# Kernel tuning notes

Hardware: AMD Instinct MI355X
Metric: run time of the kernel (lower is better)

The kernel has to match this reference:

```python
import jax, jax.numpy as jnp
import numpy as np

N_USERS = 100000
N_ITEMS = 50000
N_NODES = N_USERS + N_ITEMS
EMB = 64
NNZ = 6000000
N_LAYERS = 3


def setup_inputs() -> dict:
    key = jax.random.key(0)
    k1, k2, k3, k4, k5 = jax.random.split(key, 5)
    user_emb = jax.random.normal(k1, (N_USERS, EMB), dtype=jnp.float32) * 0.1
    item_emb = jax.random.normal(k2, (N_ITEMS, EMB), dtype=jnp.float32) * 0.1
    adj_rows = jax.random.randint(k3, (NNZ,), 0, N_NODES, dtype=jnp.int32)
    adj_cols = jax.random.randint(k4, (NNZ,), 0, N_NODES, dtype=jnp.int32)
    # normalized adjacency values (positive, small, like 1/sqrt(d_i d_j))
    adj_vals = jax.random.uniform(k5, (NNZ,), dtype=jnp.float32) * 0.05
    return {"user_emb": user_emb, "item_emb": item_emb,
            "adj_rows": adj_rows, "adj_cols": adj_cols, "adj_vals": adj_vals}


def _spmm(rows, cols, vals, x):
    # sparse [N,N] @ dense [N,D] via gather + segment_sum
    msgs = vals[:, None] * x[cols]                      # [nnz, D]
    return jax.ops.segment_sum(msgs, rows, num_segments=N_NODES)


def reference(user_emb, item_emb, adj_rows, adj_cols, adj_vals):
    emb = jnp.concatenate([user_emb, item_emb], axis=0)  # [N, D]
    all_emb = [emb]
    for _ in range(N_LAYERS):
        emb = _spmm(adj_rows, adj_cols, adj_vals, emb)
        all_emb.append(emb)
    stacked = jnp.stack(all_emb)                         # [L+1, N, D]
    final_emb = stacked.mean(axis=0)                     # [N, D]
    return (final_emb[:N_USERS], final_emb[N_USERS:], stacked)
```

## Files before the change

### kernel.cpp

```cpp
#include <hip/hip_runtime.h>
#include <hip/hip_bf16.h>


constexpr int N_USERS = 100000;
constexpr int N_ITEMS = 50000;
constexpr int N_NODES = N_USERS + N_ITEMS;
constexpr int EMB     = 64;
constexpr int NNZ     = 6000000;
constexpr long long NODE_ELEMS = (long long)N_NODES * EMB;
constexpr float SCALE     = 64.0f;
constexpr float INV_SCALE = 1.0f / 64.0f;
constexpr float VMAX      = 0.05f;
constexpr float VENC      = 16383.0f / VMAX;
constexpr float VDEC      = VMAX / 16383.0f;

constexpr int BSHIFT = 10;
constexpr int BROWS  = 1 << BSHIFT;
constexpr int NBUCK  = (N_NODES + BROWS - 1) / BROWS;

constexpr int COPY_BLOCKS = (int)((NODE_ELEMS / 4 + 255) / 256);
constexpr int HIST_EPT = 16;
constexpr int HIST_BLOCKS = (NNZ + 256 * HIST_EPT - 1) / (256 * HIST_EPT);

__device__ __forceinline__ unsigned int enc_fp8x4(float a, float b, float c, float d) {
    int r = 0;
    r = __builtin_amdgcn_cvt_pk_fp8_f32(a, b, r, false);
    r = __builtin_amdgcn_cvt_pk_fp8_f32(c, d, r, true);
    return (unsigned int)r;
}
__device__ __forceinline__ float4 dec_fp8x4(unsigned int u) {
    auto lo = __builtin_amdgcn_cvt_pk_f32_fp8((int)u, false);
    auto hi = __builtin_amdgcn_cvt_pk_f32_fp8((int)u, true);
    return make_float4(lo[0], lo[1], hi[0], hi[1]);
}

__global__ void zero_buckets_kernel(int* __restrict__ p) {
    int t = threadIdx.x;
    if (t < NBUCK) p[t] = 0;
}

__global__ void copy_hist_kernel(const float* __restrict__ user_emb,
                                 const float* __restrict__ item_emb,
                                 float* __restrict__ slot0,
                                 unsigned int* __restrict__ xq0,
                                 const int* __restrict__ rows,
                                 int* __restrict__ bucket_cnt) {
    if (blockIdx.x < COPY_BLOCKS) {
        long long i4 = (long long)blockIdx.x * 256 + threadIdx.x;
        long long n4 = NODE_ELEMS / 4;
        if (i4 >= n4) return;
        long long i = i4 * 4;
        const long long user_elems = (long long)N_USERS * EMB;
        float4 v;
        if (i < user_elems) {
            v = *reinterpret_cast<const float4*>(user_emb + i);
        } else {
            v = *reinterpret_cast<const float4*>(item_emb + (i - user_elems));
        }
        *reinterpret_cast<float4*>(slot0 + i) = v;
        xq0[i4] = enc_fp8x4(v.x * SCALE, v.y * SCALE, v.z * SCALE, v.w * SCALE);
    } else {
        __shared__ int lcnt[NBUCK];
        int bid = blockIdx.x - COPY_BLOCKS;
        int tid = threadIdx.x;
        for (int i = tid; i < NBUCK; i += 256) lcnt[i] = 0;
        __syncthreads();
        long long base = (long long)bid * 256 * HIST_EPT;
        for (int k = 0; k < HIST_EPT; ++k) {
            long long e = base + (long long)k * 256 + tid;
            if (e < NNZ) atomicAdd(&lcnt[rows[e] >> BSHIFT], 1);
        }
        __syncthreads();
        for (int i = tid; i < NBUCK; i += 256) {
            int c = lcnt[i];
            if (c) atomicAdd(&bucket_cnt[i], c);
        }
    }
}

__global__ void bucket_scan_kernel(const int* __restrict__ bucket_cnt,
                                   int* __restrict__ bucket_base,
                                   int* __restrict__ bucket_cursor,
                                   int* __restrict__ row_ptr) {
    __shared__ int s[256];
    int t = threadIdx.x;
    s[t] = (t < NBUCK) ? bucket_cnt[t] : 0;
    __syncthreads();
    int orig = s[t];
    for (int off = 1; off < 256; off <<= 1) {
        int v = (t >= off) ? s[t - off] : 0;
        __syncthreads();
        s[t] += v;
        __syncthreads();
    }
    int excl = s[t] - orig;
    if (t < NBUCK) {
        bucket_base[t] = excl;
        bucket_cursor[t] = excl;
    }
    if (t == NBUCK - 1) bucket_base[NBUCK] = s[t];
    if (t == 0) row_ptr[N_NODES] = NNZ;
}

constexpr int PART_T   = 1024;
constexpr int PART_EPT = 16;
__global__ __launch_bounds__(PART_T) void partition_kernel(
        const int* __restrict__ rows,
        const int* __restrict__ cols,
        const float* __restrict__ vals,
        int* __restrict__ bucket_cursor,
        unsigned long long* __restrict__ part) {
    __shared__ int lcnt[NBUCK];
    __shared__ int lcur[NBUCK];
    int tid = threadIdx.x;
    for (int i = tid; i < NBUCK; i += PART_T) lcnt[i] = 0;
    __syncthreads();
    long long tbase = (long long)blockIdx.x * PART_T * PART_EPT;
    int rloc[PART_EPT];
#pragma unroll
    for (int k = 0; k < PART_EPT; ++k) {
        long long e = tbase + (long long)k * PART_T + tid;
        int r = (e < NNZ) ? rows[e] : -1;
        rloc[k] = r;
        if (r >= 0) atomicAdd(&lcnt[r >> BSHIFT], 1);
    }
    __syncthreads();
    for (int i = tid; i < NBUCK; i += PART_T) {
        lcur[i] = atomicAdd(&bucket_cursor[i], lcnt[i]);
    }
    __syncthreads();
#pragma unroll
    for (int k = 0; k < PART_EPT; ++k) {
        int r = rloc[k];
        if (r < 0) continue;
        long long e = tbase + (long long)k * PART_T + tid;
        int b = r >> BSHIFT;
        int pos = atomicAdd(&lcur[b], 1);
        unsigned int w0 = ((unsigned int)(r & (BROWS - 1)) << 18) | (unsigned int)cols[e];
        unsigned int q = (unsigned int)(int)(fminf(fmaxf(vals[e] * VENC + 0.5f, 0.0f), 16383.0f));
        part[pos] = ((unsigned long long)q << 32) | (unsigned long long)w0;
    }
}

__global__ __launch_bounds__(BROWS) void bucket_sort_kernel(
        const int* __restrict__ bucket_base,
        const unsigned long long* __restrict__ part,
        int* __restrict__ row_ptr,
        unsigned int* __restrict__ col_val) {
    __shared__ int lcnt[BROWS];
    __shared__ int lcur[BROWS];
    int b = blockIdx.x;
    int t = threadIdx.x;
    int base = bucket_base[b];
    int n    = bucket_base[b + 1] - base;
    lcnt[t] = 0;
    __syncthreads();
    for (int j = t; j < n; j += BROWS) {
        unsigned int w0 = (unsigned int)part[base + j];
        atomicAdd(&lcnt[w0 >> 18], 1);
    }
    __syncthreads();
    int orig = lcnt[t];
    for (int off = 1; off < BROWS; off <<= 1) {
        int v = (t >= off) ? lcnt[t - off] : 0;
        __syncthreads();
        lcnt[t] += v;
        __syncthreads();
    }
    int excl = lcnt[t] - orig;
    int gr = b * BROWS + t;
    if (gr < N_NODES) row_ptr[gr] = base + excl;
    lcur[t] = base + excl;
    __syncthreads();
    for (int j = t; j < n; j += BROWS) {
        unsigned long long w = part[base + j];
        unsigned int w0 = (unsigned int)w;
        unsigned int q  = (unsigned int)(w >> 32);
        int rowoff = (int)(w0 >> 18);
        unsigned int col = w0 & 0x3FFFFu;
        int pos = atomicAdd(&lcur[rowoff], 1);
        col_val[pos] = (col << 14) | q;
    }
}

__global__ void spmm_fp8_kernel(const int* __restrict__ row_ptr,
                                const unsigned int* __restrict__ col_val,
                                const unsigned int* __restrict__ xq_in,
                                float* __restrict__ y,
                                unsigned int* __restrict__ xq_out,
                                const float4* __restrict__ s0,
                                const float4* __restrict__ s1,
                                const float4* __restrict__ s2,
                                float4* __restrict__ fin) {
    int row = blockIdx.x * (blockDim.x >> 6) + (threadIdx.x >> 6);
    int lane = threadIdx.x & 63;
    int g  = lane >> 4;
    int d4 = lane & 15;
    if (row >= N_NODES) return;
    int s = row_ptr[row];
    int e = row_ptr[row + 1];
    float4 acc = make_float4(0.f, 0.f, 0.f, 0.f);
    int i = s;
    for (; i + 32 <= e; i += 32) {
        unsigned int cv[8];
        unsigned int q[8];
#pragma unroll
        for (int k = 0; k < 8; ++k) cv[k] = col_val[i + 4 * k + g];
#pragma unroll
        for (int k = 0; k < 8; ++k) q[k] = xq_in[((cv[k] >> 14) << 4) | d4];
#pragma unroll
        for (int k = 0; k < 8; ++k) {
            float v = (float)(cv[k] & 0x3FFFu) * VDEC;
            float4 x = dec_fp8x4(q[k]);
            acc.x += v * x.x; acc.y += v * x.y; acc.z += v * x.z; acc.w += v * x.w;
        }
    }
    for (; i < e; i += 16) {
        unsigned int cv[4];
        unsigned int q[4];
#pragma unroll
        for (int k = 0; k < 4; ++k) {
            int idx = i + 4 * k + g;
            cv[k] = (idx < e) ? col_val[idx] : 0u;
        }
#pragma unroll
        for (int k = 0; k < 4; ++k) q[k] = xq_in[((cv[k] >> 14) << 4) | d4];
#pragma unroll
        for (int k = 0; k < 4; ++k) {
            float v = (float)(cv[k] & 0x3FFFu) * VDEC;
            float4 x = dec_fp8x4(q[k]);
            acc.x += v * x.x; acc.y += v * x.y; acc.z += v * x.z; acc.w += v * x.w;
        }
    }
    acc.x += __shfl_xor(acc.x, 16); acc.y += __shfl_xor(acc.y, 16);
    acc.z += __shfl_xor(acc.z, 16); acc.w += __shfl_xor(acc.w, 16);
    acc.x += __shfl_xor(acc.x, 32); acc.y += __shfl_xor(acc.y, 32);
    acc.z += __shfl_xor(acc.z, 32); acc.w += __shfl_xor(acc.w, 32);
    if (g == 0) {
        long long o = (long long)row * 16 + d4;
        float4 r;
        r.x = acc.x * INV_SCALE;
        r.y = acc.y * INV_SCALE;
        r.z = acc.z * INV_SCALE;
        r.w = acc.w * INV_SCALE;
        reinterpret_cast<float4*>(y)[o] = r;
        if (xq_out) xq_out[o] = enc_fp8x4(acc.x, acc.y, acc.z, acc.w);
        if (fin) {
            float4 a = s0[o], b = s1[o], c = s2[o];
            float4 f;
            f.x = (a.x + b.x + c.x + r.x) * 0.25f;
            f.y = (a.y + b.y + c.y + r.y) * 0.25f;
            f.z = (a.z + b.z + c.z + r.z) * 0.25f;
            f.w = (a.w + b.w + c.w + r.w) * 0.25f;
            fin[o] = f;
        }
    }
}

extern "C" void kernel_launch(void* const* d_in, const int* in_sizes, int n_in,
                              void* d_out, int out_size, void* d_ws, size_t ws_size,
                              hipStream_t stream) {
    const float* user_emb = (const float*)d_in[0];
    const float* item_emb = (const float*)d_in[1];
    const int*   adj_rows = (const int*)d_in[2];
    const int*   adj_cols = (const int*)d_in[3];
    const float* adj_vals = (const float*)d_in[4];

    float* out = (float*)d_out;
    float* final_emb = out;
    float* stacked   = out + NODE_ELEMS;
    float* slot[4];
    for (int l = 0; l < 4; ++l) slot[l] = stacked + (long long)l * NODE_ELEMS;

    unsigned long long* part = (unsigned long long*)slot[1];

    size_t off = 0;
    auto carve = [&](size_t bytes) { size_t o = off; off += (bytes + 15) & ~(size_t)15; return o; };
    size_t o_rp = carve((size_t)(N_NODES + 1) * 4);
    size_t o_cv = carve((size_t)NNZ * 4);
    size_t o_bc = carve((size_t)NBUCK * 4);
    size_t o_bb = carve((size_t)(NBUCK + 1) * 4);
    size_t o_bu = carve((size_t)NBUCK * 4);
    size_t o_x0 = carve((size_t)(NODE_ELEMS / 4) * 4);
    size_t o_x1 = carve((size_t)(NODE_ELEMS / 4) * 4);
    char* ws = (char*)d_ws;
    int*          row_ptr       = (int*)(ws + o_rp);
    unsigned int* col_val       = (unsigned int*)(ws + o_cv);
    int*          bucket_cnt    = (int*)(ws + o_bc);
    int*          bucket_base   = (int*)(ws + o_bb);
    int*          bucket_cursor = (int*)(ws + o_bu);
    unsigned int* xq[2];
    xq[0] = (unsigned int*)(ws + o_x0);
    xq[1] = (unsigned int*)(ws + o_x1);

    const int B = 256;

    zero_buckets_kernel<<<1, 256, 0, stream>>>(bucket_cnt);
    copy_hist_kernel<<<COPY_BLOCKS + HIST_BLOCKS, B, 0, stream>>>(
        user_emb, item_emb, slot[0], xq[0], adj_rows, bucket_cnt);

    bucket_scan_kernel<<<1, 256, 0, stream>>>(bucket_cnt, bucket_base, bucket_cursor, row_ptr);
    const int part_grid = (NNZ + PART_T * PART_EPT - 1) / (PART_T * PART_EPT);
    partition_kernel<<<part_grid, PART_T, 0, stream>>>(
        adj_rows, adj_cols, adj_vals, bucket_cursor, part);
    bucket_sort_kernel<<<NBUCK, BROWS, 0, stream>>>(bucket_base, part, row_ptr, col_val);

    const int rows_per_block = B / 64;
    const int grid_spmm = (N_NODES + rows_per_block - 1) / rows_per_block;
    for (int l = 0; l < 3; ++l) {
        unsigned int* xq_in  = xq[l & 1];
        unsigned int* xq_out = (l < 2) ? xq[(l + 1) & 1] : nullptr;
        bool last = (l == 2);
        spmm_fp8_kernel<<<grid_spmm, B, 0, stream>>>(
            row_ptr, col_val, xq_in, slot[l + 1], xq_out,
            last ? (const float4*)slot[0] : nullptr,
            last ? (const float4*)slot[1] : nullptr,
            last ? (const float4*)slot[2] : nullptr,
            last ? (float4*)final_emb : nullptr);
    }
}
```

Before: 479.5 us.

## Split CSR rows into column bands and run SpMM as persistent column-phased blocks

The bucket sort now orders each row's nonzeros by column band (five bands of 32K columns) and writes per-row, per-band pointers. The SpMM is replaced by a persistent kernel of 512 blocks, each owning a contiguous range of rows with accumulators in shared memory. Blocks sweep the column bands in phase, so the gathered fp8 embedding working set at any time is a fraction of the table and is meant to stay cache resident. In exchange, each row is processed in up to five short segments with reductions per segment, there is only one wave per row at a time, and load balance becomes static.

New measurement: 945.7 us. +97.2%, slower.

```diff
diff --git a/kernel.cpp b/kernel.cpp
--- a/kernel.cpp
+++ b/kernel.cpp
@@ -17,6 +17,9 @@
 constexpr int BSHIFT = 10;
 constexpr int BROWS  = 1 << BSHIFT;
 constexpr int NBUCK  = (N_NODES + BROWS - 1) / BROWS;
+
+constexpr int NQ     = 5;
+constexpr int QSHIFT = 15;
 
 constexpr int COPY_BLOCKS = (int)((NODE_ELEMS / 4 + 255) / 256);
 constexpr int HIST_EPT = 16;
@@ -81,7 +84,7 @@
 __global__ void bucket_scan_kernel(const int* __restrict__ bucket_cnt,
                                    int* __restrict__ bucket_base,
                                    int* __restrict__ bucket_cursor,
-                                   int* __restrict__ row_ptr) {
+                                   int* __restrict__ rpq) {
     __shared__ int s[256];
     int t = threadIdx.x;
     s[t] = (t < NBUCK) ? bucket_cnt[t] : 0;
@@ -99,7 +102,7 @@
         bucket_cursor[t] = excl;
     }
     if (t == NBUCK - 1) bucket_base[NBUCK] = s[t];
-    if (t == 0) row_ptr[N_NODES] = NNZ;
+    if (t == 0) rpq[(long long)N_NODES * NQ] = NNZ;
 }
 
 constexpr int PART_T   = 1024;
@@ -145,32 +148,43 @@
 __global__ __launch_bounds__(BROWS) void bucket_sort_kernel(
         const int* __restrict__ bucket_base,
         const unsigned long long* __restrict__ part,
-        int* __restrict__ row_ptr,
+        int* __restrict__ rpq,
         unsigned int* __restrict__ col_val) {
-    __shared__ int lcnt[BROWS];
-    __shared__ int lcur[BROWS];
+    __shared__ int lcnt[BROWS * NQ];
+    __shared__ int lcur[BROWS * NQ];
+    __shared__ int ssum[BROWS];
     int b = blockIdx.x;
     int t = threadIdx.x;
     int base = bucket_base[b];
     int n    = bucket_base[b + 1] - base;
-    lcnt[t] = 0;
+    for (int i = t; i < BROWS * NQ; i += BROWS) lcnt[i] = 0;
     __syncthreads();
     for (int j = t; j < n; j += BROWS) {
         unsigned int w0 = (unsigned int)part[base + j];
-        atomicAdd(&lcnt[w0 >> 18], 1);
-    }
-    __syncthreads();
-    int orig = lcnt[t];
+        int rowoff = (int)(w0 >> 18);
+        unsigned int col = w0 & 0x3FFFFu;
+        atomicAdd(&lcnt[rowoff * NQ + (col >> QSHIFT)], 1);
+    }
+    __syncthreads();
+    int local = 0;
+#pragma unroll
+    for (int qq = 0; qq < NQ; ++qq) local += lcnt[t * NQ + qq];
+    ssum[t] = local;
+    __syncthreads();
     for (int off = 1; off < BROWS; off <<= 1) {
-        int v = (t >= off) ? lcnt[t - off] : 0;
-        __syncthreads();
-        lcnt[t] += v;
-        __syncthreads();
-    }
-    int excl = lcnt[t] - orig;
+        int v = (t >= off) ? ssum[t - off] : 0;
+        __syncthreads();
+        ssum[t] += v;
+        __syncthreads();
+    }
+    int run = base + ((t == 0) ? 0 : ssum[t - 1]);
     int gr = b * BROWS + t;
-    if (gr < N_NODES) row_ptr[gr] = base + excl;
-    lcur[t] = base + excl;
+#pragma unroll
+    for (int qq = 0; qq < NQ; ++qq) {
+        if (gr < N_NODES) rpq[(long long)gr * NQ + qq] = run;
+        lcur[t * NQ + qq] = run;
+        run += lcnt[t * NQ + qq];
+    }
     __syncthreads();
     for (int j = t; j < n; j += BROWS) {
         unsigned long long w = part[base + j];
@@ -178,80 +192,96 @@
         unsigned int q  = (unsigned int)(w >> 32);
         int rowoff = (int)(w0 >> 18);
         unsigned int col = w0 & 0x3FFFFu;
-        int pos = atomicAdd(&lcur[rowoff], 1);
+        int pos = atomicAdd(&lcur[rowoff * NQ + (col >> QSHIFT)], 1);
         col_val[pos] = (col << 14) | q;
     }
 }
 
-__global__ void spmm_fp8_kernel(const int* __restrict__ row_ptr,
-                                const unsigned int* __restrict__ col_val,
-                                const unsigned int* __restrict__ xq_in,
-                                float* __restrict__ y,
-                                unsigned int* __restrict__ xq_out,
-                                const float4* __restrict__ s0,
-                                const float4* __restrict__ s1,
-                                const float4* __restrict__ s2,
-                                float4* __restrict__ fin) {
-    int row = blockIdx.x * (blockDim.x >> 6) + (threadIdx.x >> 6);
-    int lane = threadIdx.x & 63;
-    int g  = lane >> 4;
-    int d4 = lane & 15;
-    if (row >= N_NODES) return;
-    int s = row_ptr[row];
-    int e = row_ptr[row + 1];
-    float4 acc = make_float4(0.f, 0.f, 0.f, 0.f);
-    int i = s;
-    for (; i + 32 <= e; i += 32) {
-        unsigned int cv[8];
-        unsigned int q[8];
-#pragma unroll
-        for (int k = 0; k < 8; ++k) cv[k] = col_val[i + 4 * k + g];
-#pragma unroll
-        for (int k = 0; k < 8; ++k) q[k] = xq_in[((cv[k] >> 14) << 4) | d4];
-#pragma unroll
-        for (int k = 0; k < 8; ++k) {
-            float v = (float)(cv[k] & 0x3FFFu) * VDEC;
-            float4 x = dec_fp8x4(q[k]);
-            acc.x += v * x.x; acc.y += v * x.y; acc.z += v * x.z; acc.w += v * x.w;
-        }
-    }
-    for (; i < e; i += 16) {
-        unsigned int cv[4];
-        unsigned int q[4];
-#pragma unroll
-        for (int k = 0; k < 4; ++k) {
-            int idx = i + 4 * k + g;
-            cv[k] = (idx < e) ? col_val[idx] : 0u;
-        }
-#pragma unroll
-        for (int k = 0; k < 4; ++k) q[k] = xq_in[((cv[k] >> 14) << 4) | d4];
-#pragma unroll
-        for (int k = 0; k < 4; ++k) {
-            float v = (float)(cv[k] & 0x3FFFu) * VDEC;
-            float4 x = dec_fp8x4(q[k]);
-            acc.x += v * x.x; acc.y += v * x.y; acc.z += v * x.z; acc.w += v * x.w;
-        }
-    }
-    acc.x += __shfl_xor(acc.x, 16); acc.y += __shfl_xor(acc.y, 16);
-    acc.z += __shfl_xor(acc.z, 16); acc.w += __shfl_xor(acc.w, 16);
-    acc.x += __shfl_xor(acc.x, 32); acc.y += __shfl_xor(acc.y, 32);
-    acc.z += __shfl_xor(acc.z, 32); acc.w += __shfl_xor(acc.w, 32);
-    if (g == 0) {
-        long long o = (long long)row * 16 + d4;
-        float4 r;
-        r.x = acc.x * INV_SCALE;
-        r.y = acc.y * INV_SCALE;
-        r.z = acc.z * INV_SCALE;
-        r.w = acc.w * INV_SCALE;
-        reinterpret_cast<float4*>(y)[o] = r;
-        if (xq_out) xq_out[o] = enc_fp8x4(acc.x, acc.y, acc.z, acc.w);
+constexpr int SPMM_BLOCKS = 512;
+constexpr int SPMM_T      = 512;
+constexpr int ROWS_PB     = (N_NODES + SPMM_BLOCKS - 1) / SPMM_BLOCKS;
+constexpr int ROWS_PW     = (ROWS_PB + 7) / 8;
+
+#define FMA4(A, V, X) \
+    A.x += (V) * (X).x; A.y += (V) * (X).y; A.z += (V) * (X).z; A.w += (V) * (X).w;
+
+__global__ __launch_bounds__(SPMM_T) void spmm_persist_kernel(
+        const int* __restrict__ rpq,
+        const unsigned int* __restrict__ col_val,
+        const unsigned int* __restrict__ xq_in,
+        float* __restrict__ y,
+        unsigned int* __restrict__ xq_out,
+        const float4* __restrict__ s0,
+        const float4* __restrict__ s1,
+        const float4* __restrict__ s2,
+        float4* __restrict__ fin) {
+    __shared__ float yacc[ROWS_PB * EMB];
+    int tid = threadIdx.x;
+    for (int i = tid; i < ROWS_PB * EMB; i += SPMM_T) yacc[i] = 0.f;
+    __syncthreads();
+
+    int w    = tid >> 6;
+    int lane = tid & 63;
+    int g    = lane >> 4;
+    int d4   = lane & 15;
+    int rb   = blockIdx.x * ROWS_PB;
+    int rl0  = w * ROWS_PW;
+    int rl1  = rl0 + ROWS_PW; if (rl1 > ROWS_PB) rl1 = ROWS_PB;
+
+    for (int q = 0; q < NQ; ++q) {
+        for (int rl = rl0; rl < rl1; ++rl) {
+            int r = rb + rl;
+            if (r >= N_NODES) break;
+            int i = rpq[(long long)r * NQ + q];
+            int e = rpq[(long long)r * NQ + q + 1];
+            if (i >= e) continue;
+            float4 acc = make_float4(0.f, 0.f, 0.f, 0.f);
+            for (; i < e; i += 16) {
+                unsigned int cv[4], qq[4];
+#pragma unroll
+                for (int k = 0; k < 4; ++k) {
+                    int idx = i + 4 * k + g;
+                    cv[k] = (idx < e) ? col_val[idx] : 0u;
+                }
+#pragma unroll
+                for (int k = 0; k < 4; ++k) qq[k] = xq_in[((cv[k] >> 14) << 4) | d4];
+#pragma unroll
+                for (int k = 0; k < 4; ++k) {
+                    float v = (float)(cv[k] & 0x3FFFu) * VDEC;
+                    float4 x = dec_fp8x4(qq[k]);
+                    FMA4(acc, v, x);
+                }
+            }
+            acc.x += __shfl_xor(acc.x, 16); acc.y += __shfl_xor(acc.y, 16);
+            acc.z += __shfl_xor(acc.z, 16); acc.w += __shfl_xor(acc.w, 16);
+            acc.x += __shfl_xor(acc.x, 32); acc.y += __shfl_xor(acc.y, 32);
+            acc.z += __shfl_xor(acc.z, 32); acc.w += __shfl_xor(acc.w, 32);
+            if (g == 0) {
+                float4* p = reinterpret_cast<float4*>(&yacc[rl * EMB + d4 * 4]);
+                float4 o = *p;
+                o.x += acc.x; o.y += acc.y; o.z += acc.z; o.w += acc.w;
+                *p = o;
+            }
+        }
+    }
+
+    for (int rl = rl0 + g; rl < rl1; rl += 4) {
+        int r = rb + rl;
+        if (r >= N_NODES) continue;
+        float4 v = *reinterpret_cast<float4*>(&yacc[rl * EMB + d4 * 4]);
+        long long o = (long long)r * 16 + d4;
+        float4 rr;
+        rr.x = v.x * INV_SCALE; rr.y = v.y * INV_SCALE;
+        rr.z = v.z * INV_SCALE; rr.w = v.w * INV_SCALE;
+        reinterpret_cast<float4*>(y)[o] = rr;
+        if (xq_out) xq_out[o] = enc_fp8x4(v.x, v.y, v.z, v.w);
         if (fin) {
             float4 a = s0[o], b = s1[o], c = s2[o];
             float4 f;
-            f.x = (a.x + b.x + c.x + r.x) * 0.25f;
-            f.y = (a.y + b.y + c.y + r.y) * 0.25f;
-            f.z = (a.z + b.z + c.z + r.z) * 0.25f;
-            f.w = (a.w + b.w + c.w + r.w) * 0.25f;
+            f.x = (a.x + b.x + c.x + rr.x) * 0.25f;
+            f.y = (a.y + b.y + c.y + rr.y) * 0.25f;
+            f.z = (a.z + b.z + c.z + rr.z) * 0.25f;
+            f.w = (a.w + b.w + c.w + rr.w) * 0.25f;
             fin[o] = f;
         }
     }
@@ -276,7 +306,7 @@
 
     size_t off = 0;
     auto carve = [&](size_t bytes) { size_t o = off; off += (bytes + 15) & ~(size_t)15; return o; };
-    size_t o_rp = carve((size_t)(N_NODES + 1) * 4);
+    size_t o_rp = carve(((size_t)N_NODES * NQ + 1) * 4);
     size_t o_cv = carve((size_t)NNZ * 4);
     size_t o_bc = carve((size_t)NBUCK * 4);
     size_t o_bb = carve((size_t)(NBUCK + 1) * 4);
@@ -284,7 +314,7 @@
     size_t o_x0 = carve((size_t)(NODE_ELEMS / 4) * 4);
     size_t o_x1 = carve((size_t)(NODE_ELEMS / 4) * 4);
     char* ws = (char*)d_ws;
-    int*          row_ptr       = (int*)(ws + o_rp);
+    int*          rpq           = (int*)(ws + o_rp);
     unsigned int* col_val       = (unsigned int*)(ws + o_cv);
     int*          bucket_cnt    = (int*)(ws + o_bc);
     int*          bucket_base   = (int*)(ws + o_bb);
@@ -299,20 +329,18 @@
     copy_hist_kernel<<<COPY_BLOCKS + HIST_BLOCKS, B, 0, stream>>>(
         user_emb, item_emb, slot[0], xq[0], adj_rows, bucket_cnt);
 
-    bucket_scan_kernel<<<1, 256, 0, stream>>>(bucket_cnt, bucket_base, bucket_cursor, row_ptr);
+    bucket_scan_kernel<<<1, 256, 0, stream>>>(bucket_cnt, bucket_base, bucket_cursor, rpq);
     const int part_grid = (NNZ + PART_T * PART_EPT - 1) / (PART_T * PART_EPT);
     partition_kernel<<<part_grid, PART_T, 0, stream>>>(
         adj_rows, adj_cols, adj_vals, bucket_cursor, part);
-    bucket_sort_kernel<<<NBUCK, BROWS, 0, stream>>>(bucket_base, part, row_ptr, col_val);
-
-    const int rows_per_block = B / 64;
-    const int grid_spmm = (N_NODES + rows_per_block - 1) / rows_per_block;
+    bucket_sort_kernel<<<NBUCK, BROWS, 0, stream>>>(bucket_base, part, rpq, col_val);
+
     for (int l = 0; l < 3; ++l) {
         unsigned int* xq_in  = xq[l & 1];
         unsigned int* xq_out = (l < 2) ? xq[(l + 1) & 1] : nullptr;
         bool last = (l == 2);
-        spmm_fp8_kernel<<<grid_spmm, B, 0, stream>>>(
-            row_ptr, col_val, xq_in, slot[l + 1], xq_out,
+        spmm_persist_kernel<<<SPMM_BLOCKS, SPMM_T, 0, stream>>>(
+            rpq, col_val, xq_in, slot[l + 1], xq_out,
             last ? (const float4*)slot[0] : nullptr,
             last ? (const float4*)slot[1] : nullptr,
             last ? (const float4*)slot[2] : nullptr,
```
